# Kernel optimization log

Hardware: AMD Instinct MI355X
Metric: run time of the kernel (lower is better)

The kernel has to match this reference:

```python
import jax, jax.numpy as jnp
import numpy as np

N_NODES = 50000
N_EDGES = 640000
IN_SIZE = 512
HID1 = 128


def setup_inputs() -> dict:
    key = jax.random.key(0)
    ks = jax.random.split(key, 7)
    x = jax.random.normal(ks[0], (N_NODES, IN_SIZE), dtype=jnp.float32)
    edge_index = jax.random.randint(ks[1], (2, N_EDGES), 0, N_NODES, dtype=jnp.int64)
    # Linear params stored as (in, out) so y = x @ W + b (equiv to torch x @ W.T + b)
    s_enc = 1.0 / np.sqrt(IN_SIZE)
    s_dec = 1.0 / np.sqrt(HID1)
    W_enc = jax.random.uniform(ks[2], (IN_SIZE, HID1), jnp.float32, -s_enc, s_enc)
    b_enc = jax.random.uniform(ks[3], (HID1,), jnp.float32, -s_enc, s_enc)
    W_dec = jax.random.uniform(ks[4], (HID1, IN_SIZE), jnp.float32, -s_dec, s_dec)
    b_dec = jax.random.uniform(ks[5], (IN_SIZE,), jnp.float32, -s_dec, s_dec)
    gcn_bias = jnp.zeros((HID1,), dtype=jnp.float32)  # reset_parameters zeroes it
    return {"x": x, "W_enc": W_enc, "b_enc": b_enc, "W_dec": W_dec,
            "b_dec": b_dec, "gcn_bias": gcn_bias, "edge_index": edge_index}


def gcn_conv(h, edge_index, bias):
    # GCNConv with lin.weight frozen to identity (in==out), so lin is a no-op.
    N = h.shape[0]
    loops = jnp.arange(N, dtype=edge_index.dtype)
    row = jnp.concatenate([edge_index[0], loops])  # source nodes (x_j)
    col = jnp.concatenate([edge_index[1], loops])  # target nodes (aggregation)
    deg = jax.ops.segment_sum(jnp.ones_like(col, dtype=h.dtype), col, num_segments=N)
    dinv = jnp.where(deg > 0, jax.lax.rsqrt(deg), jnp.zeros_like(deg))
    norm = dinv[row] * dinv[col]              # [E+N]
    msg = norm[:, None] * h[row]              # gather + scale, [E+N, HID1]
    out = jax.ops.segment_sum(msg, col, num_segments=N)  # scatter-add
    return out + bias


def reference(x, W_enc, b_enc, W_dec, b_dec, gcn_bias, edge_index):
    encoded = jax.nn.relu(x @ W_enc + b_enc)          # [N, HID1]
    messaged = gcn_conv(encoded, edge_index, gcn_bias)
    decoded = jax.nn.sigmoid(messaged @ W_dec + b_dec)  # [N, IN_SIZE]
    return decoded
```

## Files before the change

### kernel.cpp

```cpp
#include <hip/hip_runtime.h>
#include <math.h>

#define NNODES 50000
#define NEDGES 640000
#define INSZ 512
#define HID 128
#define NBLK ((NNODES + 255) / 256)

typedef short s16x8 __attribute__((ext_vector_type(8)));
typedef float f32x4 __attribute__((ext_vector_type(4)));

static __device__ inline short f2bf(float f) {
    __bf16 b = (__bf16)f;
    return __builtin_bit_cast(short, b);
}
static __device__ inline float bf2f(unsigned short u) {
    unsigned int i = (unsigned int)u << 16;
    return __builtin_bit_cast(float, i);
}

__global__ __launch_bounds__(256) void prep_wenc(const float* __restrict__ W,
                                                 short* __restrict__ WT) {
    int t = blockIdx.x * 256 + threadIdx.x;
    if (t < INSZ * HID) {
        int n = t & (HID - 1);
        int k = t >> 7;
        WT[n * INSZ + k] = f2bf(W[t]);
    }
}
__global__ __launch_bounds__(256) void prep_wdec(const float* __restrict__ W,
                                                 short* __restrict__ WT) {
    int t = blockIdx.x * 256 + threadIdx.x;
    if (t < HID * INSZ) {
        int n = t & (INSZ - 1);
        int k = t >> 9;
        WT[n * HID + k] = f2bf(W[t]);
    }
}

__global__ __launch_bounds__(256) void count_kernel(const int* __restrict__ col,
                                                    int* __restrict__ counts) {
    int e = blockIdx.x * blockDim.x + threadIdx.x;
    if (e < NEDGES) atomicAdd(&counts[col[e]], 1);
}

__global__ __launch_bounds__(256) void partial_kernel(const int* __restrict__ counts,
                                                      int* __restrict__ blocksums) {
    int i = blockIdx.x * 256 + threadIdx.x;
    int v = (i < NNODES) ? counts[i] : 0;
#pragma unroll
    for (int off = 32; off; off >>= 1) v += __shfl_down(v, off, 64);
    __shared__ int ws[4];
    if ((threadIdx.x & 63) == 0) ws[threadIdx.x >> 6] = v;
    __syncthreads();
    if (threadIdx.x == 0) blocksums[blockIdx.x] = ws[0] + ws[1] + ws[2] + ws[3];
}

__global__ __launch_bounds__(256) void scan_blocks(const int* __restrict__ blocksums,
                                                   int* __restrict__ blockoffs) {
    __shared__ int s[256];
    const int t = threadIdx.x;
    s[t] = (t < NBLK) ? blocksums[t] : 0;
    __syncthreads();
    for (int off = 1; off < 256; off <<= 1) {
        int u = (t >= off) ? s[t - off] : 0;
        __syncthreads();
        s[t] += u;
        __syncthreads();
    }
    blockoffs[t] = (t == 0) ? 0 : s[t - 1];
}

__global__ __launch_bounds__(256) void scan_final(const int* __restrict__ counts,
                                                  const int* __restrict__ blockoffs,
                                                  int* __restrict__ starts,
                                                  int* __restrict__ cursor,
                                                  float* __restrict__ dinv) {
    __shared__ int s[256];
    const int t = threadIdx.x;
    const int i = blockIdx.x * 256 + t;
    int v = (i < NNODES) ? counts[i] : 0;
    s[t] = v;
    __syncthreads();
    for (int off = 1; off < 256; off <<= 1) {
        int u = (t >= off) ? s[t - off] : 0;
        __syncthreads();
        s[t] += u;
        __syncthreads();
    }
    int excl = ((t == 0) ? 0 : s[t - 1]) + blockoffs[blockIdx.x];
    if (i < NNODES) {
        starts[i] = excl;
        cursor[i] = excl;
        dinv[i] = rsqrtf((float)v + 1.0f);
        if (i == NNODES - 1) starts[NNODES] = excl + v;
    }
}

__global__ __launch_bounds__(256) void scatter_kernel(const int* __restrict__ erow,
                                                      const int* __restrict__ ecol,
                                                      int* __restrict__ cursor,
                                                      int* __restrict__ csr_row) {
    int e = blockIdx.x * blockDim.x + threadIdx.x;
    if (e < NEDGES) {
        int pos = atomicAdd(&cursor[ecol[e]], 1);
        csr_row[pos] = erow[e];
    }
}

#define XPAD 72
__global__ __launch_bounds__(256) void encoder_mfma(const float* __restrict__ x,
                                                    const short* __restrict__ WT,
                                                    const float* __restrict__ b,
                                                    unsigned short* __restrict__ h) {
    __shared__ short xs[2][32 * XPAD];
    const int t    = threadIdx.x;
    const int lane = t & 63;
    const int wv   = t >> 6;
    const int r16  = lane & 15;
    const int kg   = lane >> 4;
    const int mbase = blockIdx.x * 32;
    const int nb    = wv * 32;

    const float4* sp[2];
    int sdst[2];
#pragma unroll
    for (int j = 0; j < 2; ++j) {
        int c = j * 256 + t;
        int row = c >> 4, c4 = c & 15;
        int gr = mbase + row; if (gr >= NNODES) gr = NNODES - 1;
        sp[j]   = (const float4*)x + (size_t)gr * (INSZ / 4) + c4;
        sdst[j] = row * XPAD + c4 * 4;
    }

    f32x4 acc[2][2] = {};
    float4 rB[2], rC[2];

    {
        float4 rA[2];
#pragma unroll
        for (int j = 0; j < 2; ++j) rA[j] = sp[j][0];
#pragma unroll
        for (int j = 0; j < 2; ++j) {
            short4 w;
            w.x = f2bf(rA[j].x); w.y = f2bf(rA[j].y);
            w.z = f2bf(rA[j].z); w.w = f2bf(rA[j].w);
            *(short4*)&xs[0][sdst[j]] = w;
        }
    }
    __syncthreads();
#pragma unroll
    for (int j = 0; j < 2; ++j) rB[j] = sp[j][16];

#pragma unroll 2
    for (int ks = 0; ks < 8; ++ks) {
        const int cur = ks & 1;
        if (ks < 6) {
#pragma unroll
            for (int j = 0; j < 2; ++j) rC[j] = sp[j][(ks + 2) * 16];
        }
#pragma unroll
        for (int kk = 0; kk < 2; ++kk) {
            s16x8 a[2], bb[2];
#pragma unroll
            for (int mt = 0; mt < 2; ++mt)
                a[mt] = *(const s16x8*)&xs[cur][(mt * 16 + r16) * XPAD + kk * 32 + kg * 8];
#pragma unroll
            for (int nt = 0; nt < 2; ++nt)
                bb[nt] = *(const s16x8*)(WT + (size_t)(nb + nt * 16 + r16) * INSZ + ks * 64 + kk * 32 + kg * 8);
#pragma unroll
            for (int mt = 0; mt < 2; ++mt)
#pragma unroll
                for (int nt = 0; nt < 2; ++nt)
                    acc[mt][nt] = __builtin_amdgcn_mfma_f32_16x16x32_bf16(a[mt], bb[nt], acc[mt][nt], 0, 0, 0);
        }
        if (ks < 7) {
#pragma unroll
            for (int j = 0; j < 2; ++j) {
                short4 w;
                w.x = f2bf(rB[j].x); w.y = f2bf(rB[j].y);
                w.z = f2bf(rB[j].z); w.w = f2bf(rB[j].w);
                *(short4*)&xs[cur ^ 1][sdst[j]] = w;
            }
#pragma unroll
            for (int j = 0; j < 2; ++j) rB[j] = rC[j];
        }
        __syncthreads();
    }

    const int ro = kg * 4;
#pragma unroll
    for (int mt = 0; mt < 2; ++mt) {
        const int row0 = mbase + mt * 16 + ro;
#pragma unroll
        for (int nt = 0; nt < 2; ++nt) {
            const int col = nb + nt * 16 + r16;
            const float bj = b[col];
#pragma unroll
            for (int v = 0; v < 4; ++v) {
                int rr = row0 + v;
                if (rr < NNODES)
                    h[(size_t)rr * HID + col] = (unsigned short)f2bf(fmaxf(acc[mt][nt][v] + bj, 0.0f));
            }
        }
    }
}

__global__ __launch_bounds__(256) void aggregate_csr_kernel(const int* __restrict__ starts,
                                                            const int* __restrict__ csr_row,
                                                            const float* __restrict__ dinv,
                                                            const unsigned short* __restrict__ h,
                                                            unsigned short* __restrict__ agg) {
    const int node = (blockIdx.x * 256 + threadIdx.x) >> 5;
    const int l32  = threadIdx.x & 31;
    if (node >= NNODES) return;
    const float dc = dinv[node];
    const int s0 = starts[node], s1 = starts[node + 1];
    const ushort4* hp = (const ushort4*)h;

    ushort4 sv = hp[(size_t)node * 32 + l32];
    const float sc = dc * dc;
    float4 acc;
    acc.x = bf2f(sv.x) * sc; acc.y = bf2f(sv.y) * sc;
    acc.z = bf2f(sv.z) * sc; acc.w = bf2f(sv.w) * sc;

    int i = s0;
    for (; i + 3 < s1; i += 4) {
        int r0 = csr_row[i], r1 = csr_row[i + 1], r2 = csr_row[i + 2], r3 = csr_row[i + 3];
        float n0 = dinv[r0] * dc, n1 = dinv[r1] * dc, n2 = dinv[r2] * dc, n3 = dinv[r3] * dc;
        ushort4 h0 = hp[(size_t)r0 * 32 + l32];
        ushort4 h1 = hp[(size_t)r1 * 32 + l32];
        ushort4 h2 = hp[(size_t)r2 * 32 + l32];
        ushort4 h3 = hp[(size_t)r3 * 32 + l32];
        acc.x = fmaf(n0, bf2f(h0.x), acc.x); acc.y = fmaf(n0, bf2f(h0.y), acc.y);
        acc.z = fmaf(n0, bf2f(h0.z), acc.z); acc.w = fmaf(n0, bf2f(h0.w), acc.w);
        acc.x = fmaf(n1, bf2f(h1.x), acc.x); acc.y = fmaf(n1, bf2f(h1.y), acc.y);
        acc.z = fmaf(n1, bf2f(h1.z), acc.z); acc.w = fmaf(n1, bf2f(h1.w), acc.w);
        acc.x = fmaf(n2, bf2f(h2.x), acc.x); acc.y = fmaf(n2, bf2f(h2.y), acc.y);
        acc.z = fmaf(n2, bf2f(h2.z), acc.z); acc.w = fmaf(n2, bf2f(h2.w), acc.w);
        acc.x = fmaf(n3, bf2f(h3.x), acc.x); acc.y = fmaf(n3, bf2f(h3.y), acc.y);
        acc.z = fmaf(n3, bf2f(h3.z), acc.z); acc.w = fmaf(n3, bf2f(h3.w), acc.w);
    }
    for (; i < s1; ++i) {
        int r = csr_row[i];
        float nrm = dinv[r] * dc;
        ushort4 hv = hp[(size_t)r * 32 + l32];
        acc.x = fmaf(nrm, bf2f(hv.x), acc.x); acc.y = fmaf(nrm, bf2f(hv.y), acc.y);
        acc.z = fmaf(nrm, bf2f(hv.z), acc.z); acc.w = fmaf(nrm, bf2f(hv.w), acc.w);
    }
    ushort4 ov;
    ov.x = (unsigned short)f2bf(acc.x); ov.y = (unsigned short)f2bf(acc.y);
    ov.z = (unsigned short)f2bf(acc.z); ov.w = (unsigned short)f2bf(acc.w);
    ((ushort4*)agg)[(size_t)node * 32 + l32] = ov;
}

#define APAD 136
#define EPAD 68
__global__ __launch_bounds__(512) void decoder_mfma(const unsigned short* __restrict__ agg,
                                                    const float* __restrict__ gb,
                                                    const short* __restrict__ WT,
                                                    const float* __restrict__ b,
                                                    float* __restrict__ out) {
    __shared__ short as_lds[64 * APAD];
    __shared__ float ep[8][16 * EPAD];
    const int t    = threadIdx.x;
    const int lane = t & 63;
    const int wv   = t >> 6;
    const int r16  = lane & 15;
    const int kg   = lane >> 4;
    const int mbase = blockIdx.x * 64;
    const int nwb   = wv * 64;

    {
        const int row = t >> 3;
        const int f0  = (t & 7) * 16;
        int gr = mbase + row; if (gr >= NNODES) gr = NNODES - 1;
        const ushort4* src4 = (const ushort4*)(agg + (size_t)gr * HID + f0);
        const float4*  g4   = (const float4*)(gb + f0);
        short4* d4 = (short4*)(as_lds + row * APAD + f0);
#pragma unroll
        for (int j = 0; j < 4; ++j) {
            ushort4 u = src4[j];
            float4 g = g4[j];
            short4 w;
            w.x = f2bf(bf2f(u.x) + g.x); w.y = f2bf(bf2f(u.y) + g.y);
            w.z = f2bf(bf2f(u.z) + g.z); w.w = f2bf(bf2f(u.w) + g.w);
            d4[j] = w;
        }
    }
    __syncthreads();

    f32x4 acc[4][4] = {};
#pragma unroll
    for (int ks = 0; ks < 4; ++ks) {
        s16x8 a[4], bb[4];
#pragma unroll
        for (int mt = 0; mt < 4; ++mt)
            a[mt] = *(const s16x8*)&as_lds[(mt * 16 + r16) * APAD + ks * 32 + kg * 8];
#pragma unroll
        for (int nt = 0; nt < 4; ++nt)
            bb[nt] = *(const s16x8*)(WT + (size_t)(nwb + nt * 16 + r16) * HID + ks * 32 + kg * 8);
#pragma unroll
        for (int mt = 0; mt < 4; ++mt)
#pragma unroll
            for (int nt = 0; nt < 4; ++nt)
                acc[mt][nt] = __builtin_amdgcn_mfma_f32_16x16x32_bf16(a[mt], bb[nt], acc[mt][nt], 0, 0, 0);
    }

    float bj[4];
#pragma unroll
    for (int nt = 0; nt < 4; ++nt) bj[nt] = b[nwb + nt * 16 + r16];

    float* eps = ep[wv];
#pragma unroll
    for (int mt = 0; mt < 4; ++mt) {
#pragma unroll
        for (int nt = 0; nt < 4; ++nt)
#pragma unroll
            for (int v = 0; v < 4; ++v) {
                float z = acc[mt][nt][v] + bj[nt];
                eps[(kg * 4 + v) * EPAD + nt * 16 + r16] = 1.0f / (1.0f + __expf(-z));
            }
#pragma unroll
        for (int pass = 0; pass < 4; ++pass) {
            const int lr = pass * 4 + kg;
            float4 vv = *(const float4*)&eps[lr * EPAD + r16 * 4];
            const int rr = mbase + mt * 16 + lr;
            if (rr < NNODES)
                *(float4*)&out[(size_t)rr * INSZ + nwb + r16 * 4] = vv;
        }
    }
}

extern "C" void kernel_launch(void* const* d_in, const int* in_sizes, int n_in,
                              void* d_out, int out_size, void* d_ws, size_t ws_size,
                              hipStream_t stream) {
    const float* x        = (const float*)d_in[0];
    const float* W_enc    = (const float*)d_in[1];
    const float* b_enc    = (const float*)d_in[2];
    const float* W_dec    = (const float*)d_in[3];
    const float* b_dec    = (const float*)d_in[4];
    const float* gcn_bias = (const float*)d_in[5];
    const int*   edge     = (const int*)d_in[6];
    const int*   erow = edge;
    const int*   ecol = edge + NEDGES;

    float* out = (float*)d_out;
    unsigned short* agg = (unsigned short*)d_ws;
    float* dinv  = (float*)(agg + (size_t)NNODES * HID);
    short* wdecT = (short*)(dinv + NNODES);
    unsigned short* h = (unsigned short*)out;
    int*   csr_row   = (int*)(out + (size_t)NNODES * HID);
    int*   starts    = csr_row + NEDGES;
    int*   counts    = starts + NNODES + 1;
    int*   cursor    = counts + NNODES;
    int*   blocksums = cursor + NNODES;
    int*   blockoffs = blocksums + 256;
    short* wencT     = (short*)(blockoffs + 256);

    hipMemsetAsync(counts, 0, (size_t)NNODES * sizeof(int), stream);
    prep_wenc<<<(INSZ * HID + 255) / 256, 256, 0, stream>>>(W_enc, wencT);
    prep_wdec<<<(HID * INSZ + 255) / 256, 256, 0, stream>>>(W_dec, wdecT);
    count_kernel<<<(NEDGES + 255) / 256, 256, 0, stream>>>(ecol, counts);
    partial_kernel<<<NBLK, 256, 0, stream>>>(counts, blocksums);
    scan_blocks<<<1, 256, 0, stream>>>(blocksums, blockoffs);
    scan_final<<<NBLK, 256, 0, stream>>>(counts, blockoffs, starts, cursor, dinv);
    scatter_kernel<<<(NEDGES + 255) / 256, 256, 0, stream>>>(erow, ecol, cursor, csr_row);
    encoder_mfma<<<(NNODES + 31) / 32, 256, 0, stream>>>(x, wencT, b_enc, h);
    aggregate_csr_kernel<<<((size_t)NNODES * 32 + 255) / 256, 256, 0, stream>>>(starts, csr_row, dinv, h, agg);
    decoder_mfma<<<(NNODES + 63) / 64, 512, 0, stream>>>(agg, gcn_bias, wdecT, b_dec, out);
}
```

Baseline: 193.5 us.

## Fuse CSR aggregation into decoder and degree counting into encoder

The separate CSR gather-aggregation kernel is folded into the decoder prologue, so each decoder block aggregates its 64 nodes straight into LDS instead of writing and re-reading an intermediate agg buffer. The edge-degree count atomics move into the encoder kernel as a grid-stride loop, removing one launch. This cuts two launches and an HBM round trip for the aggregated features. In exchange the decoder prologue is longer and more irregular, which can lower decoder occupancy and overlap. The workspace layout is reorganised so h lives in workspace rather than the output buffer.

After: 228.5 us. 1.18x slower.

```diff
diff --git a/kernel.cpp b/kernel.cpp
--- a/kernel.cpp
+++ b/kernel.cpp
@@ -36,12 +36,6 @@
         int k = t >> 9;
         WT[n * HID + k] = f2bf(W[t]);
     }
-}
-
-__global__ __launch_bounds__(256) void count_kernel(const int* __restrict__ col,
-                                                    int* __restrict__ counts) {
-    int e = blockIdx.x * blockDim.x + threadIdx.x;
-    if (e < NEDGES) atomicAdd(&counts[col[e]], 1);
 }
 
 __global__ __launch_bounds__(256) void partial_kernel(const int* __restrict__ counts,
@@ -112,7 +106,9 @@
 __global__ __launch_bounds__(256) void encoder_mfma(const float* __restrict__ x,
                                                     const short* __restrict__ WT,
                                                     const float* __restrict__ b,
-                                                    unsigned short* __restrict__ h) {
+                                                    unsigned short* __restrict__ h,
+                                                    const int* __restrict__ ecol,
+                                                    int* __restrict__ counts) {
     __shared__ short xs[2][32 * XPAD];
     const int t    = threadIdx.x;
     const int lane = t & 63;
@@ -122,6 +118,9 @@
     const int mbase = blockIdx.x * 32;
     const int nb    = wv * 32;
 
+    for (int e = blockIdx.x * 256 + t; e < NEDGES; e += gridDim.x * 256)
+        atomicAdd(&counts[ecol[e]], 1);
+
     const float4* sp[2];
     int sdst[2];
 #pragma unroll
@@ -206,61 +205,16 @@
     }
 }
 
-__global__ __launch_bounds__(256) void aggregate_csr_kernel(const int* __restrict__ starts,
-                                                            const int* __restrict__ csr_row,
-                                                            const float* __restrict__ dinv,
-                                                            const unsigned short* __restrict__ h,
-                                                            unsigned short* __restrict__ agg) {
-    const int node = (blockIdx.x * 256 + threadIdx.x) >> 5;
-    const int l32  = threadIdx.x & 31;
-    if (node >= NNODES) return;
-    const float dc = dinv[node];
-    const int s0 = starts[node], s1 = starts[node + 1];
-    const ushort4* hp = (const ushort4*)h;
-
-    ushort4 sv = hp[(size_t)node * 32 + l32];
-    const float sc = dc * dc;
-    float4 acc;
-    acc.x = bf2f(sv.x) * sc; acc.y = bf2f(sv.y) * sc;
-    acc.z = bf2f(sv.z) * sc; acc.w = bf2f(sv.w) * sc;
-
-    int i = s0;
-    for (; i + 3 < s1; i += 4) {
-        int r0 = csr_row[i], r1 = csr_row[i + 1], r2 = csr_row[i + 2], r3 = csr_row[i + 3];
-        float n0 = dinv[r0] * dc, n1 = dinv[r1] * dc, n2 = dinv[r2] * dc, n3 = dinv[r3] * dc;
-        ushort4 h0 = hp[(size_t)r0 * 32 + l32];
-        ushort4 h1 = hp[(size_t)r1 * 32 + l32];
-        ushort4 h2 = hp[(size_t)r2 * 32 + l32];
-        ushort4 h3 = hp[(size_t)r3 * 32 + l32];
-        acc.x = fmaf(n0, bf2f(h0.x), acc.x); acc.y = fmaf(n0, bf2f(h0.y), acc.y);
-        acc.z = fmaf(n0, bf2f(h0.z), acc.z); acc.w = fmaf(n0, bf2f(h0.w), acc.w);
-        acc.x = fmaf(n1, bf2f(h1.x), acc.x); acc.y = fmaf(n1, bf2f(h1.y), acc.y);
-        acc.z = fmaf(n1, bf2f(h1.z), acc.z); acc.w = fmaf(n1, bf2f(h1.w), acc.w);
-        acc.x = fmaf(n2, bf2f(h2.x), acc.x); acc.y = fmaf(n2, bf2f(h2.y), acc.y);
-        acc.z = fmaf(n2, bf2f(h2.z), acc.z); acc.w = fmaf(n2, bf2f(h2.w), acc.w);
-        acc.x = fmaf(n3, bf2f(h3.x), acc.x); acc.y = fmaf(n3, bf2f(h3.y), acc.y);
-        acc.z = fmaf(n3, bf2f(h3.z), acc.z); acc.w = fmaf(n3, bf2f(h3.w), acc.w);
-    }
-    for (; i < s1; ++i) {
-        int r = csr_row[i];
-        float nrm = dinv[r] * dc;
-        ushort4 hv = hp[(size_t)r * 32 + l32];
-        acc.x = fmaf(nrm, bf2f(hv.x), acc.x); acc.y = fmaf(nrm, bf2f(hv.y), acc.y);
-        acc.z = fmaf(nrm, bf2f(hv.z), acc.z); acc.w = fmaf(nrm, bf2f(hv.w), acc.w);
-    }
-    ushort4 ov;
-    ov.x = (unsigned short)f2bf(acc.x); ov.y = (unsigned short)f2bf(acc.y);
-    ov.z = (unsigned short)f2bf(acc.z); ov.w = (unsigned short)f2bf(acc.w);
-    ((ushort4*)agg)[(size_t)node * 32 + l32] = ov;
-}
-
 #define APAD 136
 #define EPAD 68
-__global__ __launch_bounds__(512) void decoder_mfma(const unsigned short* __restrict__ agg,
-                                                    const float* __restrict__ gb,
-                                                    const short* __restrict__ WT,
-                                                    const float* __restrict__ b,
-                                                    float* __restrict__ out) {
+__global__ __launch_bounds__(512) void decoder_fused(const int* __restrict__ starts,
+                                                     const int* __restrict__ csr_row,
+                                                     const float* __restrict__ dinv,
+                                                     const unsigned short* __restrict__ h,
+                                                     const float* __restrict__ gb,
+                                                     const short* __restrict__ WT,
+                                                     const float* __restrict__ b,
+                                                     float* __restrict__ out) {
     __shared__ short as_lds[64 * APAD];
     __shared__ float ep[8][16 * EPAD];
     const int t    = threadIdx.x;
@@ -272,20 +226,51 @@
     const int nwb   = wv * 64;
 
     {
-        const int row = t >> 3;
-        const int f0  = (t & 7) * 16;
-        int gr = mbase + row; if (gr >= NNODES) gr = NNODES - 1;
-        const ushort4* src4 = (const ushort4*)(agg + (size_t)gr * HID + f0);
-        const float4*  g4   = (const float4*)(gb + f0);
-        short4* d4 = (short4*)(as_lds + row * APAD + f0);
-#pragma unroll
-        for (int j = 0; j < 4; ++j) {
-            ushort4 u = src4[j];
-            float4 g = g4[j];
+        const int hw  = t >> 5;
+        const int l32 = t & 31;
+        const ushort4* hp = (const ushort4*)h;
+        const float4 gbv = *(const float4*)(gb + l32 * 4);
+#pragma unroll
+        for (int pass = 0; pass < 4; ++pass) {
+            const int nl = hw + pass * 16;
+            const int node = mbase + nl;
+            float4 acc = make_float4(0.f, 0.f, 0.f, 0.f);
+            if (node < NNODES) {
+                const float dc = dinv[node];
+                const int s0 = starts[node], s1 = starts[node + 1];
+                ushort4 sv = hp[(size_t)node * 32 + l32];
+                const float sc = dc * dc;
+                acc.x = bf2f(sv.x) * sc; acc.y = bf2f(sv.y) * sc;
+                acc.z = bf2f(sv.z) * sc; acc.w = bf2f(sv.w) * sc;
+                int i = s0;
+                for (; i + 3 < s1; i += 4) {
+                    int r0 = csr_row[i], r1 = csr_row[i + 1], r2 = csr_row[i + 2], r3 = csr_row[i + 3];
+                    float n0 = dinv[r0] * dc, n1 = dinv[r1] * dc, n2 = dinv[r2] * dc, n3 = dinv[r3] * dc;
+                    ushort4 h0 = hp[(size_t)r0 * 32 + l32];
+                    ushort4 h1 = hp[(size_t)r1 * 32 + l32];
+                    ushort4 h2 = hp[(size_t)r2 * 32 + l32];
+                    ushort4 h3 = hp[(size_t)r3 * 32 + l32];
+                    acc.x = fmaf(n0, bf2f(h0.x), acc.x); acc.y = fmaf(n0, bf2f(h0.y), acc.y);
+                    acc.z = fmaf(n0, bf2f(h0.z), acc.z); acc.w = fmaf(n0, bf2f(h0.w), acc.w);
+                    acc.x = fmaf(n1, bf2f(h1.x), acc.x); acc.y = fmaf(n1, bf2f(h1.y), acc.y);
+                    acc.z = fmaf(n1, bf2f(h1.z), acc.z); acc.w = fmaf(n1, bf2f(h1.w), acc.w);
+                    acc.x = fmaf(n2, bf2f(h2.x), acc.x); acc.y = fmaf(n2, bf2f(h2.y), acc.y);
+                    acc.z = fmaf(n2, bf2f(h2.z), acc.z); acc.w = fmaf(n2, bf2f(h2.w), acc.w);
+                    acc.x = fmaf(n3, bf2f(h3.x), acc.x); acc.y = fmaf(n3, bf2f(h3.y), acc.y);
+                    acc.z = fmaf(n3, bf2f(h3.z), acc.z); acc.w = fmaf(n3, bf2f(h3.w), acc.w);
+                }
+                for (; i < s1; ++i) {
+                    int r = csr_row[i];
+                    float nrm = dinv[r] * dc;
+                    ushort4 hv = hp[(size_t)r * 32 + l32];
+                    acc.x = fmaf(nrm, bf2f(hv.x), acc.x); acc.y = fmaf(nrm, bf2f(hv.y), acc.y);
+                    acc.z = fmaf(nrm, bf2f(hv.z), acc.z); acc.w = fmaf(nrm, bf2f(hv.w), acc.w);
+                }
+            }
             short4 w;
-            w.x = f2bf(bf2f(u.x) + g.x); w.y = f2bf(bf2f(u.y) + g.y);
-            w.z = f2bf(bf2f(u.z) + g.z); w.w = f2bf(bf2f(u.w) + g.w);
-            d4[j] = w;
+            w.x = f2bf(acc.x + gbv.x); w.y = f2bf(acc.y + gbv.y);
+            w.z = f2bf(acc.z + gbv.z); w.w = f2bf(acc.w + gbv.w);
+            *(short4*)&as_lds[nl * APAD + l32 * 4] = w;
         }
     }
     __syncthreads();
@@ -346,27 +331,25 @@
     const int*   ecol = edge + NEDGES;
 
     float* out = (float*)d_out;
-    unsigned short* agg = (unsigned short*)d_ws;
-    float* dinv  = (float*)(agg + (size_t)NNODES * HID);
-    short* wdecT = (short*)(dinv + NNODES);
-    unsigned short* h = (unsigned short*)out;
-    int*   csr_row   = (int*)(out + (size_t)NNODES * HID);
+    unsigned short* h = (unsigned short*)d_ws;
+    float* dinv      = (float*)(h + (size_t)NNODES * HID);
+    short* wencT     = (short*)(dinv + NNODES);
+    short* wdecT     = wencT + INSZ * HID;
+    int*   csr_row   = (int*)(wdecT + HID * INSZ);
     int*   starts    = csr_row + NEDGES;
     int*   counts    = starts + NNODES + 1;
     int*   cursor    = counts + NNODES;
     int*   blocksums = cursor + NNODES;
     int*   blockoffs = blocksums + 256;
-    short* wencT     = (short*)(blockoffs + 256);
 
     hipMemsetAsync(counts, 0, (size_t)NNODES * sizeof(int), stream);
     prep_wenc<<<(INSZ * HID + 255) / 256, 256, 0, stream>>>(W_enc, wencT);
     prep_wdec<<<(HID * INSZ + 255) / 256, 256, 0, stream>>>(W_dec, wdecT);
-    count_kernel<<<(NEDGES + 255) / 256, 256, 0, stream>>>(ecol, counts);
+    encoder_mfma<<<(NNODES + 31) / 32, 256, 0, stream>>>(x, wencT, b_enc, h, ecol, counts);
     partial_kernel<<<NBLK, 256, 0, stream>>>(counts, blocksums);
     scan_blocks<<<1, 256, 0, stream>>>(blocksums, blockoffs);
     scan_final<<<NBLK, 256, 0, stream>>>(counts, blockoffs, starts, cursor, dinv);
     scatter_kernel<<<(NEDGES + 255) / 256, 256, 0, stream>>>(erow, ecol, cursor, csr_row);
-    encoder_mfma<<<(NNODES + 31) / 32, 256, 0, stream>>>(x, wencT, b_enc, h);
-    aggregate_csr_kernel<<<((size_t)NNODES * 32 + 255) / 256, 256, 0, stream>>>(starts, csr_row, dinv, h, agg);
-    decoder_mfma<<<(NNODES + 63) / 64, 512, 0, stream>>>(agg, gcn_bias, wdecT, b_dec, out);
-}
+    decoder_fused<<<(NNODES + 63) / 64, 512, 0, stream>>>(starts, csr_row, dinv, h,
+                                                          gcn_bias, wdecT, b_dec, out);
+}
```
